# Optimization experiments

Measured on AMD Instinct MI355X. Metric: run time of the kernel, lower is better.

Reference implementation:

```python
import jax, jax.numpy as jnp
import numpy as np

N = 50000      # nodes
E = 800000     # edges (avg degree 16)
F_IN = 64      # node_feature_space
H = 64         # hidden_dim
G = 16         # graphs in batch
BN_EPS = 1e-5


def setup_inputs() -> dict:
    key = jax.random.key(0)
    ks = jax.random.split(key, 8)
    x = jax.random.normal(ks[0], (N, F_IN), jnp.float32)
    edge_index = jax.random.randint(ks[1], (2, E), 0, N, dtype=jnp.int64)
    batch = jnp.sort(jax.random.randint(ks[2], (N,), 0, G, dtype=jnp.int64))
    init = lambda k, shp, fan: jax.random.normal(k, shp, jnp.float32) / np.float32(np.sqrt(fan))
    params = dict(
        W1_0=init(ks[3], (F_IN, H), F_IN), b1_0=jnp.zeros((H,), jnp.float32),
        W2_0=init(ks[4], (H, H), H),       b2_0=jnp.zeros((H,), jnp.float32),
        g_0=jnp.ones((H,), jnp.float32),   be_0=jnp.zeros((H,), jnp.float32),
        W1_1=init(ks[5], (H, H), H),       b1_1=jnp.zeros((H,), jnp.float32),
        W2_1=init(ks[6], (H, H), H),       b2_1=jnp.zeros((H,), jnp.float32),
        g_1=jnp.ones((H,), jnp.float32),   be_1=jnp.zeros((H,), jnp.float32),
    )
    return dict(x=x, edge_index=edge_index, batch=batch, **params)


def _gin_layer(x, src, dst, W1, b1, W2, b2, g, be):
    # GINConv (eps=0): h_i = MLP(x_i + sum_{j->i} x_j)
    agg = jax.ops.segment_sum(x[src], dst, num_segments=N)   # [N, d]
    h = x + agg
    h = jnp.maximum(h @ W1 + b1, 0.0) @ W2 + b2              # Linear-ReLU-Linear
    # BatchNorm1d (training-mode batch stats, biased variance as in torch)
    mu = h.mean(axis=0)
    var = h.var(axis=0)
    h = (h - mu) * jax.lax.rsqrt(var + BN_EPS) * g + be
    return jnp.maximum(h, 0.0)                               # ReLU


def reference(x, edge_index, batch,
              W1_0, b1_0, W2_0, b2_0, g_0, be_0,
              W1_1, b1_1, W2_1, b2_1, g_1, be_1):
    src, dst = edge_index[0], edge_index[1]
    x = _gin_layer(x, src, dst, W1_0, b1_0, W2_0, b2_0, g_0, be_0)
    x = _gin_layer(x, src, dst, W1_1, b1_1, W2_1, b2_1, g_1, be_1)
    # global_mean_pool over graph ids
    cnt = jax.ops.segment_sum(jnp.ones((N,), x.dtype), batch, num_segments=G)
    sums = jax.ops.segment_sum(x, batch, num_segments=G)
    h_graph = sums / jnp.maximum(cnt, 1.0)[:, None]
    return (x, h_graph)
```

## Files before the change

kernel.cpp:

```cpp
#include <hip/hip_runtime.h>
#include <hip/hip_bf16.h>


constexpr int NN = 50000;
constexpr int NE = 800000;
constexpr int HD = 64;
constexpr int NG = 16;
constexpr float BN_EPS = 1e-5f;
constexpr int ROWCAP = 64;

__global__ __launch_bounds__(256)
void prep_kernel(const float* __restrict__ x, __hip_bfloat16* __restrict__ xb,
                 int* __restrict__ cnt, float* __restrict__ stats0,
                 float* __restrict__ stats1, float* __restrict__ psums) {
    int i4 = blockIdx.x * 256 + threadIdx.x;
    if (i4 < NN) cnt[i4] = 0;
    if (blockIdx.x == 0) {
        if (threadIdx.x < 128) stats0[threadIdx.x] = 0.f;
        else stats1[threadIdx.x - 128] = 0.f;
    } else if (blockIdx.x == 1) {
        *(float4*)(psums + threadIdx.x * 4) = make_float4(0.f, 0.f, 0.f, 0.f);
    }
    if (i4 >= NN * HD / 4) return;
    float4 v = *(const float4*)(x + (size_t)i4 * 4);
    union { ushort4 u; __hip_bfloat16 b[4]; } p;
    p.b[0] = __float2bfloat16(v.x);
    p.b[1] = __float2bfloat16(v.y);
    p.b[2] = __float2bfloat16(v.z);
    p.b[3] = __float2bfloat16(v.w);
    *(ushort4*)((unsigned short*)xb + (size_t)i4 * 4) = p.u;
}

__global__ __launch_bounds__(256)
void scatter_kernel(const int* __restrict__ ei, int* __restrict__ cnt,
                    int* __restrict__ csr) {
    int e4 = (blockIdx.x * 256 + threadIdx.x) * 4;
    if (e4 >= NE) return;
    int4 s = *(const int4*)(ei + e4);
    int4 d = *(const int4*)(ei + NE + e4);
    int slot;
    slot = atomicAdd(&cnt[d.x], 1); if (slot < ROWCAP) csr[(d.x << 6) + slot] = s.x;
    slot = atomicAdd(&cnt[d.y], 1); if (slot < ROWCAP) csr[(d.y << 6) + slot] = s.y;
    slot = atomicAdd(&cnt[d.z], 1); if (slot < ROWCAP) csr[(d.z << 6) + slot] = s.z;
    slot = atomicAdd(&cnt[d.w], 1); if (slot < ROWCAP) csr[(d.w << 6) + slot] = s.w;
}

__global__ __launch_bounds__(256)
void agg_kernel(const float* __restrict__ x, const __hip_bfloat16* __restrict__ xb,
                const int* __restrict__ cnt, const int* __restrict__ csr,
                float* __restrict__ h) {
    int row = blockIdx.x * 4 + (threadIdx.x >> 6);
    int lane = threadIdx.x & 63;
    int m = min(cnt[row], ROWCAP);
    int ids = csr[(row << 6) + lane];
    float acc = x[(size_t)row * HD + lane];
    int j = 0;
    float a0 = 0.f, a1 = 0.f, a2 = 0.f, a3 = 0.f;
    float a4 = 0.f, a5 = 0.f, a6 = 0.f, a7 = 0.f;
    for (; j + 8 <= m; j += 8) {
        int nb0 = __shfl(ids, j);
        int nb1 = __shfl(ids, j + 1);
        int nb2 = __shfl(ids, j + 2);
        int nb3 = __shfl(ids, j + 3);
        int nb4 = __shfl(ids, j + 4);
        int nb5 = __shfl(ids, j + 5);
        int nb6 = __shfl(ids, j + 6);
        int nb7 = __shfl(ids, j + 7);
        a0 += __bfloat162float(xb[(size_t)nb0 * HD + lane]);
        a1 += __bfloat162float(xb[(size_t)nb1 * HD + lane]);
        a2 += __bfloat162float(xb[(size_t)nb2 * HD + lane]);
        a3 += __bfloat162float(xb[(size_t)nb3 * HD + lane]);
        a4 += __bfloat162float(xb[(size_t)nb4 * HD + lane]);
        a5 += __bfloat162float(xb[(size_t)nb5 * HD + lane]);
        a6 += __bfloat162float(xb[(size_t)nb6 * HD + lane]);
        a7 += __bfloat162float(xb[(size_t)nb7 * HD + lane]);
    }
    acc += ((a0 + a1) + (a2 + a3)) + ((a4 + a5) + (a6 + a7));
    for (; j < m; j++) {
        int nb = __shfl(ids, j);
        acc += __bfloat162float(xb[(size_t)nb * HD + lane]);
    }
    h[(size_t)row * HD + lane] = acc;
}

__global__ __launch_bounds__(256)
void aggn_kernel(const float* __restrict__ hraw, const __hip_bfloat16* __restrict__ xbr,
                 const int* __restrict__ cnt, const int* __restrict__ csr,
                 const float* __restrict__ stats_prev, const float* __restrict__ g0,
                 const float* __restrict__ be0, float* __restrict__ h) {
    int row = blockIdx.x * 4 + (threadIdx.x >> 6);
    int lane = threadIdx.x & 63;
    const float inv = 1.f / (float)NN;
    float mu = stats_prev[lane] * inv;
    float var = stats_prev[64 + lane] * inv - mu * mu;
    float sc = g0[lane] * rsqrtf(var + BN_EPS);
    float off = be0[lane] - mu * sc;
    int m = min(cnt[row], ROWCAP);
    int ids = csr[(row << 6) + lane];
    float acc = fmaxf(fmaf(hraw[(size_t)row * HD + lane], sc, off), 0.f);
    int j = 0;
    float a0 = 0.f, a1 = 0.f, a2 = 0.f, a3 = 0.f;
    float a4 = 0.f, a5 = 0.f, a6 = 0.f, a7 = 0.f;
    for (; j + 8 <= m; j += 8) {
        int nb0 = __shfl(ids, j);
        int nb1 = __shfl(ids, j + 1);
        int nb2 = __shfl(ids, j + 2);
        int nb3 = __shfl(ids, j + 3);
        int nb4 = __shfl(ids, j + 4);
        int nb5 = __shfl(ids, j + 5);
        int nb6 = __shfl(ids, j + 6);
        int nb7 = __shfl(ids, j + 7);
        float v0 = __bfloat162float(xbr[(size_t)nb0 * HD + lane]);
        float v1 = __bfloat162float(xbr[(size_t)nb1 * HD + lane]);
        float v2 = __bfloat162float(xbr[(size_t)nb2 * HD + lane]);
        float v3 = __bfloat162float(xbr[(size_t)nb3 * HD + lane]);
        float v4 = __bfloat162float(xbr[(size_t)nb4 * HD + lane]);
        float v5 = __bfloat162float(xbr[(size_t)nb5 * HD + lane]);
        float v6 = __bfloat162float(xbr[(size_t)nb6 * HD + lane]);
        float v7 = __bfloat162float(xbr[(size_t)nb7 * HD + lane]);
        a0 += fmaxf(fmaf(v0, sc, off), 0.f);
        a1 += fmaxf(fmaf(v1, sc, off), 0.f);
        a2 += fmaxf(fmaf(v2, sc, off), 0.f);
        a3 += fmaxf(fmaf(v3, sc, off), 0.f);
        a4 += fmaxf(fmaf(v4, sc, off), 0.f);
        a5 += fmaxf(fmaf(v5, sc, off), 0.f);
        a6 += fmaxf(fmaf(v6, sc, off), 0.f);
        a7 += fmaxf(fmaf(v7, sc, off), 0.f);
    }
    acc += ((a0 + a1) + (a2 + a3)) + ((a4 + a5) + (a6 + a7));
    for (; j < m; j++) {
        int nb = __shfl(ids, j);
        float v = __bfloat162float(xbr[(size_t)nb * HD + lane]);
        acc += fmaxf(fmaf(v, sc, off), 0.f);
    }
    h[(size_t)row * HD + lane] = acc;
}

__global__ __launch_bounds__(256)
void mlp_kernel(const float* __restrict__ hin, float* __restrict__ hout,
                const float* __restrict__ W1, const float* __restrict__ b1,
                const float* __restrict__ W2, const float* __restrict__ b2,
                float* __restrict__ stats, __hip_bfloat16* __restrict__ xbr) {
    __shared__ float sh[128 * 65];
    __shared__ float sW[64 * 64];
    __shared__ float sb[64];
    __shared__ float red[2][4][64];
    int tid = threadIdx.x;
    int base = blockIdx.x * 128;

    for (int i = tid; i < 4096; i += 256) sW[i] = W1[i];
    if (tid < 64) sb[tid] = b1[tid];
#pragma unroll
    for (int i = 0; i < 8; i++) {
        int i4 = tid + 256 * i;
        int row = i4 >> 4, col = (i4 & 15) * 4;
        int grow = base + row;
        float4 v = (grow < NN) ? *(const float4*)(hin + (size_t)grow * HD + col)
                               : make_float4(0.f, 0.f, 0.f, 0.f);
        float* d = sh + row * 65 + col;
        d[0] = v.x; d[1] = v.y; d[2] = v.z; d[3] = v.w;
    }
    __syncthreads();

    int wv = tid >> 6;
    int lane = tid & 63;

    float acc0[16], acc1[16];
#pragma unroll
    for (int j = 0; j < 16; j++) { acc0[j] = sb[wv * 16 + j]; acc1[j] = acc0[j]; }
    for (int k = 0; k < 64; k++) {
        float a0 = sh[lane * 65 + k];
        float a1 = sh[(64 + lane) * 65 + k];
        const float4* wr = (const float4*)(sW + k * 64 + wv * 16);
#pragma unroll
        for (int q = 0; q < 4; q++) {
            float4 w = wr[q];
            acc0[4 * q + 0] = fmaf(a0, w.x, acc0[4 * q + 0]);
            acc0[4 * q + 1] = fmaf(a0, w.y, acc0[4 * q + 1]);
            acc0[4 * q + 2] = fmaf(a0, w.z, acc0[4 * q + 2]);
            acc0[4 * q + 3] = fmaf(a0, w.w, acc0[4 * q + 3]);
            acc1[4 * q + 0] = fmaf(a1, w.x, acc1[4 * q + 0]);
            acc1[4 * q + 1] = fmaf(a1, w.y, acc1[4 * q + 1]);
            acc1[4 * q + 2] = fmaf(a1, w.z, acc1[4 * q + 2]);
            acc1[4 * q + 3] = fmaf(a1, w.w, acc1[4 * q + 3]);
        }
    }
    __syncthreads();

#pragma unroll
    for (int j = 0; j < 16; j++) {
        sh[lane * 65 + wv * 16 + j] = fmaxf(acc0[j], 0.f);
        sh[(64 + lane) * 65 + wv * 16 + j] = fmaxf(acc1[j], 0.f);
    }
    for (int i = tid; i < 4096; i += 256) sW[i] = W2[i];
    if (tid < 64) sb[tid] = b2[tid];
    __syncthreads();

#pragma unroll
    for (int j = 0; j < 16; j++) { acc0[j] = sb[wv * 16 + j]; acc1[j] = acc0[j]; }
    for (int k = 0; k < 64; k++) {
        float a0 = sh[lane * 65 + k];
        float a1 = sh[(64 + lane) * 65 + k];
        const float4* wr = (const float4*)(sW + k * 64 + wv * 16);
#pragma unroll
        for (int q = 0; q < 4; q++) {
            float4 w = wr[q];
            acc0[4 * q + 0] = fmaf(a0, w.x, acc0[4 * q + 0]);
            acc0[4 * q + 1] = fmaf(a0, w.y, acc0[4 * q + 1]);
            acc0[4 * q + 2] = fmaf(a0, w.z, acc0[4 * q + 2]);
            acc0[4 * q + 3] = fmaf(a0, w.w, acc0[4 * q + 3]);
            acc1[4 * q + 0] = fmaf(a1, w.x, acc1[4 * q + 0]);
            acc1[4 * q + 1] = fmaf(a1, w.y, acc1[4 * q + 1]);
            acc1[4 * q + 2] = fmaf(a1, w.z, acc1[4 * q + 2]);
            acc1[4 * q + 3] = fmaf(a1, w.w, acc1[4 * q + 3]);
        }
    }
    __syncthreads();
#pragma unroll
    for (int j = 0; j < 16; j++) {
        sh[lane * 65 + wv * 16 + j] = acc0[j];
        sh[(64 + lane) * 65 + wv * 16 + j] = acc1[j];
    }
    __syncthreads();

#pragma unroll
    for (int i = 0; i < 8; i++) {
        int i4 = tid + 256 * i;
        int row = i4 >> 4, col = (i4 & 15) * 4;
        int grow = base + row;
        if (grow < NN) {
            const float* s = sh + row * 65 + col;
            float4 v = make_float4(s[0], s[1], s[2], s[3]);
            *(float4*)(hout + (size_t)grow * HD + col) = v;
            if (xbr) {
                union { ushort4 u; __hip_bfloat16 b[4]; } p;
                p.b[0] = __float2bfloat16(v.x);
                p.b[1] = __float2bfloat16(v.y);
                p.b[2] = __float2bfloat16(v.z);
                p.b[3] = __float2bfloat16(v.w);
                *(ushort4*)((unsigned short*)xbr + (size_t)grow * HD + col) = p.u;
            }
        }
    }

    {
        int col = tid & 63;
        int r0 = (tid >> 6) * 32;
        float s = 0.f, ss = 0.f;
#pragma unroll
        for (int r = 0; r < 32; r++) {
            float v = (base + r0 + r < NN) ? sh[(r0 + r) * 65 + col] : 0.f;
            s += v;
            ss += v * v;
        }
        red[0][tid >> 6][col] = s;
        red[1][tid >> 6][col] = ss;
        __syncthreads();
        if (tid < 64) {
            float S = red[0][0][col] + red[0][1][col] + red[0][2][col] + red[0][3][col];
            atomicAdd(stats + col, S);
        } else if (tid < 128) {
            float SS = red[1][0][col] + red[1][1][col] + red[1][2][col] + red[1][3][col];
            atomicAdd(stats + 64 + col, SS);
        }
    }
}

__global__ __launch_bounds__(256)
void norm_kernel(float* h, const float* __restrict__ stats,
                 const float* __restrict__ g, const float* __restrict__ be,
                 const int* __restrict__ batch, float* __restrict__ psums) {
    __shared__ float sg[2][64];
    if (threadIdx.x < 128) sg[threadIdx.x >> 6][threadIdx.x & 63] = 0.f;
    __syncthreads();
    size_t i4 = (size_t)blockIdx.x * 256 + threadIdx.x;
    int row = (int)(i4 >> 4);
    int base_row = blockIdx.x * 16;
    int g0 = batch[base_row];
    size_t off = i4 * 4;
    int col = (int)(off & 63);
    float4 v = *(const float4*)(h + off);
    float4 sm = *(const float4*)(stats + col);
    float4 sq = *(const float4*)(stats + 64 + col);
    float4 gg = *(const float4*)(g + col);
    float4 bb = *(const float4*)(be + col);
    const float inv = 1.f / (float)NN;
    float4 o;
    {
        float mu = sm.x * inv, var = sq.x * inv - mu * mu;
        float sc = gg.x * rsqrtf(var + BN_EPS);
        o.x = fmaxf((v.x - mu) * sc + bb.x, 0.f);
    }
    {
        float mu = sm.y * inv, var = sq.y * inv - mu * mu;
        float sc = gg.y * rsqrtf(var + BN_EPS);
        o.y = fmaxf((v.y - mu) * sc + bb.y, 0.f);
    }
    {
        float mu = sm.z * inv, var = sq.z * inv - mu * mu;
        float sc = gg.z * rsqrtf(var + BN_EPS);
        o.z = fmaxf((v.z - mu) * sc + bb.z, 0.f);
    }
    {
        float mu = sm.w * inv, var = sq.w * inv - mu * mu;
        float sc = gg.w * rsqrtf(var + BN_EPS);
        o.w = fmaxf((v.w - mu) * sc + bb.w, 0.f);
    }
    *(float4*)(h + off) = o;

    int dg = batch[row] - g0;
    if (dg <= 1) {
        atomicAdd(&sg[dg][col + 0], o.x);
        atomicAdd(&sg[dg][col + 1], o.y);
        atomicAdd(&sg[dg][col + 2], o.z);
        atomicAdd(&sg[dg][col + 3], o.w);
    } else {
        int gid = g0 + dg;
        atomicAdd(&psums[gid * HD + col + 0], o.x);
        atomicAdd(&psums[gid * HD + col + 1], o.y);
        atomicAdd(&psums[gid * HD + col + 2], o.z);
        atomicAdd(&psums[gid * HD + col + 3], o.w);
    }
    __syncthreads();
    if (threadIdx.x < 128) {
        int d = threadIdx.x >> 6;
        int c = threadIdx.x & 63;
        float s = sg[d][c];
        if (g0 + d < NG && s != 0.f) atomicAdd(&psums[(g0 + d) * HD + c], s);
    }
}

__device__ __forceinline__ int lower_bound_batch(const int* __restrict__ b, int val) {
    int lo = 0, hi = NN;
    while (lo < hi) {
        int mid = (lo + hi) >> 1;
        if (b[mid] < val) lo = mid + 1;
        else hi = mid;
    }
    return lo;
}

__global__ __launch_bounds__(1024)
void pool_finalize_kernel(const float* __restrict__ sums, const int* __restrict__ batch,
                          float* __restrict__ out) {
    int g = threadIdx.x >> 6;
    int col = threadIdx.x & 63;
    int s = lower_bound_batch(batch, g);
    int e = lower_bound_batch(batch, g + 1);
    float cnt = (float)(e - s);
    out[g * HD + col] = sums[g * HD + col] / fmaxf(cnt, 1.f);
}

extern "C" void kernel_launch(void* const* d_in, const int* in_sizes, int n_in,
                              void* d_out, int out_size, void* d_ws, size_t ws_size,
                              hipStream_t stream) {
    const float* x = (const float*)d_in[0];
    const int* ei = (const int*)d_in[1];
    const int* batch = (const int*)d_in[2];
    const float* W1_0 = (const float*)d_in[3];
    const float* b1_0 = (const float*)d_in[4];
    const float* W2_0 = (const float*)d_in[5];
    const float* b2_0 = (const float*)d_in[6];
    const float* g_0 = (const float*)d_in[7];
    const float* be_0 = (const float*)d_in[8];
    const float* W1_1 = (const float*)d_in[9];
    const float* b1_1 = (const float*)d_in[10];
    const float* W2_1 = (const float*)d_in[11];
    const float* b2_1 = (const float*)d_in[12];
    const float* g_1 = (const float*)d_in[13];
    const float* be_1 = (const float*)d_in[14];

    float* out = (float*)d_out;

    float* buf_h = (float*)d_ws;
    float* stats0 = buf_h + (size_t)NN * HD;
    float* stats1 = stats0 + 128;
    float* psums = stats1 + 128;
    int* cnt = (int*)(psums + 1024);
    int* csr = cnt + NN;
    __hip_bfloat16* xb = (__hip_bfloat16*)(csr + (size_t)NN * ROWCAP);

    dim3 b256(256);
    int mlp_grid = (NN + 127) / 128;
    int norm_grid = (NN * HD / 4 + 255) / 256;
    int sct_grid = (NE / 4 + 255) / 256;
    int agg_grid = NN / 4;

    prep_kernel<<<norm_grid, b256, 0, stream>>>(x, xb, cnt, stats0, stats1, psums);
    scatter_kernel<<<sct_grid, b256, 0, stream>>>(ei, cnt, csr);

    agg_kernel<<<agg_grid, b256, 0, stream>>>(x, xb, cnt, csr, buf_h);
    mlp_kernel<<<mlp_grid, b256, 0, stream>>>(buf_h, out, W1_0, b1_0, W2_0, b2_0,
                                              stats0, xb);

    aggn_kernel<<<agg_grid, b256, 0, stream>>>(out, xb, cnt, csr,
                                               stats0, g_0, be_0, buf_h);
    mlp_kernel<<<mlp_grid, b256, 0, stream>>>(buf_h, out, W1_1, b1_1, W2_1, b2_1,
                                              stats1, (__hip_bfloat16*)nullptr);

    norm_kernel<<<norm_grid, b256, 0, stream>>>(out, stats1, g_1, be_1, batch, psums);
    pool_finalize_kernel<<<1, dim3(1024), 0, stream>>>(psums, batch, out + (size_t)NN * HD);
}
```

Measured before the change: 284.1 us.

## Partition CSR build and aggregation by destination range per XCD, use 16-bit indices

The scatter kernel now splits nodes into 8 destination partitions. Block index mod 8 picks the partition, so each XCD's blocks do the atomics and CSR writes for one contiguous node range, which keeps them in that XCD's L2. The aggregation kernels use the same block-to-partition mapping so CSR reads stay local. CSR neighbor IDs are stored as unsigned short, which halves index storage and traffic. In exchange, each scatter block reads the whole edge list 8 times and discards the edges outside its range, and the 16-bit IDs only work while N stays at or below 65535.

```diff
diff --git a/kernel.cpp b/kernel.cpp
--- a/kernel.cpp
+++ b/kernel.cpp
@@ -8,6 +8,9 @@
 constexpr int NG = 16;
 constexpr float BN_EPS = 1e-5f;
 constexpr int ROWCAP = 64;
+constexpr int NPART = 8;
+constexpr int PSZ = 6250;
+constexpr int PBLK = (PSZ + 3) / 4;
 
 __global__ __launch_bounds__(256)
 void prep_kernel(const float* __restrict__ x, __hip_bfloat16* __restrict__ xb,
@@ -33,23 +36,40 @@
 
 __global__ __launch_bounds__(256)
 void scatter_kernel(const int* __restrict__ ei, int* __restrict__ cnt,
-                    int* __restrict__ csr) {
-    int e4 = (blockIdx.x * 256 + threadIdx.x) * 4;
+                    unsigned short* __restrict__ csr) {
+    int p = blockIdx.x & 7;
+    int chunk = blockIdx.x >> 3;
+    int e4 = (chunk * 256 + threadIdx.x) * 4;
     if (e4 >= NE) return;
     int4 s = *(const int4*)(ei + e4);
     int4 d = *(const int4*)(ei + NE + e4);
+    int lo = p * PSZ, hi = lo + PSZ;
     int slot;
-    slot = atomicAdd(&cnt[d.x], 1); if (slot < ROWCAP) csr[(d.x << 6) + slot] = s.x;
-    slot = atomicAdd(&cnt[d.y], 1); if (slot < ROWCAP) csr[(d.y << 6) + slot] = s.y;
-    slot = atomicAdd(&cnt[d.z], 1); if (slot < ROWCAP) csr[(d.z << 6) + slot] = s.z;
-    slot = atomicAdd(&cnt[d.w], 1); if (slot < ROWCAP) csr[(d.w << 6) + slot] = s.w;
+    if (d.x >= lo && d.x < hi) {
+        slot = atomicAdd(&cnt[d.x], 1);
+        if (slot < ROWCAP) csr[(d.x << 6) + slot] = (unsigned short)s.x;
+    }
+    if (d.y >= lo && d.y < hi) {
+        slot = atomicAdd(&cnt[d.y], 1);
+        if (slot < ROWCAP) csr[(d.y << 6) + slot] = (unsigned short)s.y;
+    }
+    if (d.z >= lo && d.z < hi) {
+        slot = atomicAdd(&cnt[d.z], 1);
+        if (slot < ROWCAP) csr[(d.z << 6) + slot] = (unsigned short)s.z;
+    }
+    if (d.w >= lo && d.w < hi) {
+        slot = atomicAdd(&cnt[d.w], 1);
+        if (slot < ROWCAP) csr[(d.w << 6) + slot] = (unsigned short)s.w;
+    }
 }
 
 __global__ __launch_bounds__(256)
 void agg_kernel(const float* __restrict__ x, const __hip_bfloat16* __restrict__ xb,
-                const int* __restrict__ cnt, const int* __restrict__ csr,
+                const int* __restrict__ cnt, const unsigned short* __restrict__ csr,
                 float* __restrict__ h) {
-    int row = blockIdx.x * 4 + (threadIdx.x >> 6);
+    int lr = ((blockIdx.x >> 3) << 2) + (threadIdx.x >> 6);
+    if (lr >= PSZ) return;
+    int row = (blockIdx.x & 7) * PSZ + lr;
     int lane = threadIdx.x & 63;
     int m = min(cnt[row], ROWCAP);
     int ids = csr[(row << 6) + lane];
@@ -85,10 +105,12 @@
 
 __global__ __launch_bounds__(256)
 void aggn_kernel(const float* __restrict__ hraw, const __hip_bfloat16* __restrict__ xbr,
-                 const int* __restrict__ cnt, const int* __restrict__ csr,
+                 const int* __restrict__ cnt, const unsigned short* __restrict__ csr,
                  const float* __restrict__ stats_prev, const float* __restrict__ g0,
                  const float* __restrict__ be0, float* __restrict__ h) {
-    int row = blockIdx.x * 4 + (threadIdx.x >> 6);
+    int lr = ((blockIdx.x >> 3) << 2) + (threadIdx.x >> 6);
+    if (lr >= PSZ) return;
+    int row = (blockIdx.x & 7) * PSZ + lr;
     int lane = threadIdx.x & 63;
     const float inv = 1.f / (float)NN;
     float mu = stats_prev[lane] * inv;
@@ -377,14 +399,14 @@
     float* stats1 = stats0 + 128;
     float* psums = stats1 + 128;
     int* cnt = (int*)(psums + 1024);
-    int* csr = cnt + NN;
+    unsigned short* csr = (unsigned short*)(cnt + NN);
     __hip_bfloat16* xb = (__hip_bfloat16*)(csr + (size_t)NN * ROWCAP);
 
     dim3 b256(256);
     int mlp_grid = (NN + 127) / 128;
     int norm_grid = (NN * HD / 4 + 255) / 256;
-    int sct_grid = (NE / 4 + 255) / 256;
-    int agg_grid = NN / 4;
+    int sct_grid = ((NE + 1023) / 1024) * NPART;
+    int agg_grid = NPART * PBLK;
 
     prep_kernel<<<norm_grid, b256, 0, stream>>>(x, xb, cnt, stats0, stats1, psums);
     scatter_kernel<<<sct_grid, b256, 0, stream>>>(ei, cnt, csr);
```

Result: faster. 275.9 us (-2.9%).
